# Kernel optimization log

Hardware: AMD Instinct MI355X
Metric: run time of the kernel (lower is better)

Reference implementation:

```python
import jax, jax.numpy as jnp
import numpy as np

KERNEL = 7  # neighborhood window (7x7)
NUM_HEADS = 4


def _window_idx(L, k):
    # NATTEN edge-clamped window start: each query attends to exactly k neighbors.
    starts = jnp.clip(jnp.arange(L) - k // 2, 0, L - k)  # [L]
    return starts[:, None] + jnp.arange(k)[None, :]       # [L, k]


def setup_inputs() -> dict:
    key = jax.random.key(0)
    k1, k2, k3, k4, k5 = jax.random.split(key, 5)
    B, H, W, D = 8, 64, 64, 128
    return {
        "x": jax.random.normal(k1, (B, H, W, D), dtype=jnp.float32),
        "w_qkv": jax.random.normal(k2, (3 * D, D), dtype=jnp.float32) * 0.02,
        "b_qkv": jax.random.normal(k3, (3 * D,), dtype=jnp.float32) * 0.02,
        "w_proj": jax.random.normal(k4, (D, D), dtype=jnp.float32) * 0.02,
        "b_proj": jax.random.normal(k5, (D,), dtype=jnp.float32) * 0.02,
    }


def reference(x, w_qkv, b_qkv, w_proj, b_proj):
    B, H, W, D = x.shape
    nh, k = NUM_HEADS, KERNEL
    hd = D // nh
    scale = hd ** -0.5

    # QKV projection -> [3, B, nh, H, W, hd]
    qkv = x @ w_qkv.T + b_qkv
    qkv = qkv.reshape(B, H, W, 3, nh, hd).transpose(3, 0, 4, 1, 2, 5)
    q, kk, v = qkv[0], qkv[1], qkv[2]

    idx_h = _window_idx(H, k)  # [H, k]
    idx_w = _window_idx(W, k)  # [W, k]
    IH = idx_h[:, None, :, None]  # [H,1,k,1]
    IW = idx_w[None, :, None, :]  # [1,W,1,k]

    # Gather local K/V neighborhoods: [B, nh, H, W, k, k, hd] -> [B, nh, H, W, k*k, hd]
    kn = kk[:, :, IH, IW, :].reshape(B, nh, H, W, k * k, hd)
    vn = v[:, :, IH, IW, :].reshape(B, nh, H, W, k * k, hd)

    attn = jnp.einsum('bhxyd,bhxynd->bhxyn', q * scale, kn)
    attn = jax.nn.softmax(attn, axis=-1)
    out = jnp.einsum('bhxyn,bhxynd->bhxyd', attn, vn)

    out = out.transpose(0, 2, 3, 1, 4).reshape(B, H, W, D)
    return out @ w_proj.T + b_proj
```

## Files before the change

kernel.cpp:

```cpp
#include <hip/hip_runtime.h>
#include <hip/hip_bf16.h>

#define BB 8
#define HH 64
#define WW 64
#define DD 128
#define NH 4
#define HD 32
#define KS 7
#define TS 8
#define HALO 14

typedef __attribute__((ext_vector_type(8))) short short8v;
typedef __attribute__((ext_vector_type(4))) short short4v;
typedef __attribute__((ext_vector_type(4))) float f32x4;
typedef unsigned short bf16_t;

__device__ inline bf16_t f2bf(float f) {
  __hip_bfloat16 h = __float2bfloat16(f);
  return *reinterpret_cast<bf16_t*>(&h);
}

__global__ __launch_bounds__(256) void qkv_mfma(
    const float* __restrict__ x, const float* __restrict__ w,
    const float* __restrict__ bqkv,
    bf16_t* __restrict__ q, bf16_t* __restrict__ k, bf16_t* __restrict__ v) {
  __shared__ __align__(16) short smA[64 * 128];
  __shared__ __align__(16) short smB[128 * 128];
  const int tid = threadIdx.x;
  const int m_tile = blockIdx.x;
  const int n_tile = blockIdx.y;

  const float* Ab = x + (size_t)m_tile * 64 * 128;
  const float* Bb = w + (size_t)n_tile * 128 * 128;
#pragma unroll
  for (int i = 0; i < 4; i++) {
    int idx = tid + i * 256;
    int r = idx >> 4, p = idx & 15;
    const float* ap = Ab + r * 128 + p * 8;
    float4 a0 = *(const float4*)ap;
    float4 a1 = *(const float4*)(ap + 4);
    short8v s;
    s[0] = f2bf(a0.x); s[1] = f2bf(a0.y); s[2] = f2bf(a0.z); s[3] = f2bf(a0.w);
    s[4] = f2bf(a1.x); s[5] = f2bf(a1.y); s[6] = f2bf(a1.z); s[7] = f2bf(a1.w);
    *(short8v*)((char*)smA + ((r * 256 + p * 16) ^ ((r & 7) << 4))) = s;
  }
#pragma unroll
  for (int i = 0; i < 8; i++) {
    int idx = tid + i * 256;
    int r = idx >> 4, p = idx & 15;
    const float* bp_ = Bb + r * 128 + p * 8;
    float4 b0 = *(const float4*)bp_;
    float4 b1 = *(const float4*)(bp_ + 4);
    short8v t;
    t[0] = f2bf(b0.x); t[1] = f2bf(b0.y); t[2] = f2bf(b0.z); t[3] = f2bf(b0.w);
    t[4] = f2bf(b1.x); t[5] = f2bf(b1.y); t[6] = f2bf(b1.z); t[7] = f2bf(b1.w);
    *(short8v*)((char*)smB + ((r * 256 + p * 16) ^ ((r & 7) << 4))) = t;
  }
  __syncthreads();

  const int lane = tid & 63, wid = tid >> 6;
  const int wm = wid >> 1, wn = wid & 1;
  const int l15 = lane & 15, l4 = lane >> 4;

  f32x4 acc[2][4] = {};
  const int rowA0 = wm * 32 + l15;
  const int rowB0 = wn * 64 + l15;
  const int swzA = (rowA0 & 7) << 4;
  const int swzB = (rowB0 & 7) << 4;

#pragma unroll
  for (int ks = 0; ks < 4; ks++) {
    const int cb = ks * 64 + l4 * 16;
    short8v a[2], b[4];
#pragma unroll
    for (int mi = 0; mi < 2; mi++)
      a[mi] = *(const short8v*)((const char*)smA +
                ((((rowA0 + mi * 16) * 256) + cb) ^ swzA));
#pragma unroll
    for (int nj = 0; nj < 4; nj++)
      b[nj] = *(const short8v*)((const char*)smB +
                ((((rowB0 + nj * 16) * 256) + cb) ^ swzB));
#pragma unroll
    for (int mi = 0; mi < 2; mi++)
#pragma unroll
      for (int nj = 0; nj < 4; nj++)
        acc[mi][nj] = __builtin_amdgcn_mfma_f32_16x16x32_bf16(a[mi], b[nj], acc[mi][nj], 0, 0, 0);
  }

  __syncthreads();
  short* smC = smA;
  const float qscale = 0.17677669529663687f;
  const float sc = (n_tile == 0) ? qscale : 1.f;
#pragma unroll
  for (int nj = 0; nj < 4; nj++) {
    const int n_local = wn * 64 + nj * 16 + l15;
    const float bias = bqkv[n_tile * 128 + n_local];
#pragma unroll
    for (int mi = 0; mi < 2; mi++) {
#pragma unroll
      for (int r = 0; r < 4; r++) {
        const int m = wm * 32 + mi * 16 + l4 * 4 + r;
        *(bf16_t*)((char*)smC + ((m * 256 + n_local * 2) ^ ((m & 7) << 4))) =
            f2bf((acc[mi][nj][r] + bias) * sc);
      }
    }
  }
  __syncthreads();

  const int bblk = m_tile >> 6;
  bf16_t* outp = (n_tile == 0) ? q : ((n_tile == 1) ? k : v);
#pragma unroll
  for (int i = 0; i < 4; i++) {
    const int idx = i * 256 + tid;
    const int h = idx >> 8;
    const int rem = idx & 255;
    const int m = rem >> 2, c = rem & 3;
    short8v t8 = *(const short8v*)((const char*)smC +
        ((m * 256 + h * 64 + c * 16) ^ ((m & 7) << 4)));
    const int pix = (m_tile * 64 + m) & 4095;
    *(short8v*)(outp + ((size_t)(bblk * 4 + h)) * 131072 + (size_t)pix * 32 + c * 8) = t8;
  }
}

__global__ __launch_bounds__(256) void attn_mfma(
    const bf16_t* __restrict__ q, const bf16_t* __restrict__ k,
    const bf16_t* __restrict__ v, bf16_t* __restrict__ ao) {
  __shared__ __align__(16) char vtb[16384];

  const int tile = blockIdx.x;
  const int tx = tile >> 3, ty = tile & 7;
  const int head = blockIdx.y, bb = blockIdx.z;
  const size_t bh = ((size_t)bb * NH + head) * 4096;
  const bf16_t* kb = k + bh * HD;
  const bf16_t* vb = v + bh * HD;
  const bf16_t* qb = q + bh * HD;
  const int rstart = min(max(tx * TS - 3, 0), HH - HALO);
  const int cstart = min(max(ty * TS - 3, 0), WW - HALO);
  const int tid = threadIdx.x;
  const int lane = tid & 63, wid = tid >> 6;
  const int l15 = lane & 15, h4 = lane >> 4;

  short8v qf;
  int qx, qy;
  {
    const int pit = wid * 16 + l15;
    qx = tx * TS + (pit >> 3);
    qy = ty * TS + (pit & 7);
    qf = *(const short8v*)(qb + ((size_t)(qx * WW + qy)) * HD + h4 * 8);
  }
  const int wx0 = min(max(qx - 3, 0), HH - KS) - rstart;
  const int wy0 = min(max(qy - 3, 0), WW - KS) - cstart;

  const int x0 = tx * TS + wid * 2;
  const int w0 = min(max(x0 - 3, 0), HH - KS) - rstart;
  const int base = min(w0 & ~1, 4);

  short4v vl[4][2];
#pragma unroll
  for (int t = 0; t < 4; t++) {
    const int idx = tid + t * 256;
    if (idx < 784) {
      const int pp = idx >> 3, c = idx & 7;
      const int pr = pp / 7, pc2 = (pp % 7) * 2;
      const size_t g = ((size_t)((rstart + pr) * WW + (cstart + pc2))) * HD + c * 4;
      vl[t][0] = *(const short4v*)(vb + g);
      vl[t][1] = *(const short4v*)(vb + g + HD);
    }
  }

  f32x4 acc[10];
  const f32x4 zf = {0.f, 0.f, 0.f, 0.f};
  const int kcol = cstart + min(l15, 13);
#pragma unroll
  for (int ch = 0; ch < 2; ch++) {
    short8v kf[5];
#pragma unroll
    for (int i = 0; i < 5; i++) {
      const int pr = rstart + base + ch * 5 + i;
      kf[i] = *(const short8v*)(kb + ((size_t)(pr * WW + kcol)) * HD + h4 * 8);
    }
    __builtin_amdgcn_s_setprio(1);
#pragma unroll
    for (int i = 0; i < 5; i++)
      acc[ch * 5 + i] = __builtin_amdgcn_mfma_f32_16x16x32_bf16(kf[i], qf, zf, 0, 0, 0);
    __builtin_amdgcn_s_setprio(0);
  }

#pragma unroll
  for (int t = 0; t < 4; t++) {
    const int idx = tid + t * 256;
    if (idx < 784) {
      const int pp = idx >> 3, c = idx & 7;
      const int pr = pp / 7, pc2 = (pp % 7) * 2;
      const int pos0 = ((pr >> 1) << 5) + ((pc2 >> 2) << 3) + ((pr & 1) << 2) + (pc2 & 3);
#pragma unroll
      for (int j = 0; j < 4; j++) {
        const int d = c * 4 + j;
        const unsigned pk2 = (unsigned)(unsigned short)vl[t][0][j] |
                             ((unsigned)(unsigned short)vl[t][1][j] << 16);
        *(unsigned*)(vtb + ((d * 512 + pos0 * 2) ^ ((d & 7) << 4))) = pk2;
      }
    }
  }
  for (int idx = tid; idx < 512; idx += 256) {
    const int d = idx >> 4, pr = idx & 15;
    if (pr < 14) {
      const int pos = ((pr >> 1) << 5) + 24 + ((pr & 1) << 2) + 2;
      *(unsigned*)(vtb + ((d * 512 + pos * 2) ^ ((d & 7) << 4))) = 0u;
    }
  }
  __syncthreads();

  bool cv[4];
#pragma unroll
  for (int r = 0; r < 4; r++) cv[r] = ((unsigned)(h4 * 4 + r - wy0) < 7u);
  float sum = 0.f;
#pragma unroll
  for (int nt = 0; nt < 10; nt++) {
    const bool rv = ((unsigned)(base + nt - wx0) < 7u);
#pragma unroll
    for (int r = 0; r < 4; r++) {
      const float p = (rv && cv[r]) ? __expf(acc[nt][r]) : 0.f;
      acc[nt][r] = p;
      sum += p;
    }
  }
  sum += __shfl_xor(sum, 16);
  sum += __shfl_xor(sum, 32);
  const float inv = 1.f / sum;

  f32x4 o0 = zf, o1 = zf;
  const int swzv = (l15 & 7) << 4;
  const int cbase = (base >> 1) * 64;
  __builtin_amdgcn_s_setprio(1);
#pragma unroll
  for (int kc = 0; kc < 5; kc++) {
    union { unsigned u[4]; short8v s; } pa;
    pa.u[0] = (unsigned)f2bf(acc[2 * kc][0] * inv) |
              ((unsigned)f2bf(acc[2 * kc][1] * inv) << 16);
    pa.u[1] = (unsigned)f2bf(acc[2 * kc][2] * inv) |
              ((unsigned)f2bf(acc[2 * kc][3] * inv) << 16);
    pa.u[2] = (unsigned)f2bf(acc[2 * kc + 1][0] * inv) |
              ((unsigned)f2bf(acc[2 * kc + 1][1] * inv) << 16);
    pa.u[3] = (unsigned)f2bf(acc[2 * kc + 1][2] * inv) |
              ((unsigned)f2bf(acc[2 * kc + 1][3] * inv) << 16);
    const int boff = cbase + kc * 64 + h4 * 16;
    short8v vb0 = *(const short8v*)(vtb + ((l15 * 512 + boff) ^ swzv));
    short8v vb1 = *(const short8v*)(vtb + (((l15 + 16) * 512 + boff) ^ swzv));
    o0 = __builtin_amdgcn_mfma_f32_16x16x32_bf16(pa.s, vb0, o0, 0, 0, 0);
    o1 = __builtin_amdgcn_mfma_f32_16x16x32_bf16(pa.s, vb1, o1, 0, 0, 0);
  }
  __builtin_amdgcn_s_setprio(0);

#pragma unroll
  for (int r = 0; r < 4; r++) {
    const int pit = wid * 16 + h4 * 4 + r;
    const int x = tx * TS + (pit >> 3), y = ty * TS + (pit & 7);
    bf16_t* op = ao + ((size_t)bb * 4096 + x * WW + y) * DD + head * HD;
    op[l15]      = (bf16_t)f2bf(o0[r]);
    op[l15 + 16] = (bf16_t)f2bf(o1[r]);
  }
}

__global__ __launch_bounds__(256) void proj_mfma(
    const bf16_t* __restrict__ aob, const float* __restrict__ wp,
    const float* __restrict__ bp, float* __restrict__ out) {
  __shared__ __align__(16) char plds[49152];
  short* smA = (short*)plds;
  short* smB = (short*)(plds + 16384);
  const int tid = threadIdx.x;
  const int m_tile = blockIdx.x;

  const bf16_t* Ab = aob + (size_t)m_tile * 64 * 128;
#pragma unroll
  for (int i = 0; i < 4; i++) {
    int idx = tid + i * 256;
    int r = idx >> 4, p = idx & 15;
    short8v s = *(const short8v*)(Ab + r * 128 + p * 8);
    *(short8v*)((char*)smA + ((r * 256 + p * 16) ^ ((r & 7) << 4))) = s;
  }
#pragma unroll
  for (int i = 0; i < 8; i++) {
    int idx = tid + i * 256;
    int r = idx >> 4, p = idx & 15;
    const float* bp_ = wp + r * 128 + p * 8;
    float4 b0 = *(const float4*)bp_;
    float4 b1 = *(const float4*)(bp_ + 4);
    short8v t;
    t[0] = f2bf(b0.x); t[1] = f2bf(b0.y); t[2] = f2bf(b0.z); t[3] = f2bf(b0.w);
    t[4] = f2bf(b1.x); t[5] = f2bf(b1.y); t[6] = f2bf(b1.z); t[7] = f2bf(b1.w);
    *(short8v*)((char*)smB + ((r * 256 + p * 16) ^ ((r & 7) << 4))) = t;
  }
  __syncthreads();

  const int lane = tid & 63, wid = tid >> 6;
  const int wm = wid >> 1, wn = wid & 1;
  const int l15 = lane & 15, l4 = lane >> 4;

  f32x4 acc[2][4] = {};
  const int rowA0 = wm * 32 + l15;
  const int rowB0 = wn * 64 + l15;
  const int swzA = (rowA0 & 7) << 4;
  const int swzB = (rowB0 & 7) << 4;

#pragma unroll
  for (int ks = 0; ks < 4; ks++) {
    const int cb = ks * 64 + l4 * 16;
    short8v a[2], b[4];
#pragma unroll
    for (int mi = 0; mi < 2; mi++)
      a[mi] = *(const short8v*)((const char*)smA +
                ((((rowA0 + mi * 16) * 256) + cb) ^ swzA));
#pragma unroll
    for (int nj = 0; nj < 4; nj++)
      b[nj] = *(const short8v*)((const char*)smB +
                ((((rowB0 + nj * 16) * 256) + cb) ^ swzB));
#pragma unroll
    for (int mi = 0; mi < 2; mi++)
#pragma unroll
      for (int nj = 0; nj < 4; nj++)
        acc[mi][nj] = __builtin_amdgcn_mfma_f32_16x16x32_bf16(a[mi], b[nj], acc[mi][nj], 0, 0, 0);
  }

  __syncthreads();
  char* smC = plds + 16384;
#pragma unroll
  for (int nj = 0; nj < 4; nj++) {
    const int n = wn * 64 + nj * 16 + l15;
    const float bias = bp[n];
#pragma unroll
    for (int mi = 0; mi < 2; mi++) {
#pragma unroll
      for (int r = 0; r < 4; r++) {
        const int m = wm * 32 + mi * 16 + l4 * 4 + r;
        *(float*)(smC + ((m * 512 + n * 4) ^ ((m & 7) << 5))) = acc[mi][nj][r] + bias;
      }
    }
  }
  __syncthreads();

#pragma unroll
  for (int i = 0; i < 8; i++) {
    const int idx = i * 256 + tid;
    const int m = idx >> 5, c = idx & 31;
    float4 t = *(const float4*)(smC + ((m * 512 + c * 16) ^ ((m & 7) << 5)));
    *(float4*)(out + (size_t)(m_tile * 64 + m) * DD + c * 4) = t;
  }
}

extern "C" void kernel_launch(void* const* d_in, const int* in_sizes, int n_in,
                              void* d_out, int out_size, void* d_ws, size_t ws_size,
                              hipStream_t stream) {
  const float* x      = (const float*)d_in[0];
  const float* w_qkv  = (const float*)d_in[1];
  const float* b_qkv  = (const float*)d_in[2];
  const float* w_proj = (const float*)d_in[3];
  const float* b_proj = (const float*)d_in[4];
  float* out = (float*)d_out;

  const size_t per = (size_t)BB * NH * HH * WW * HD;
  bf16_t* q  = (bf16_t*)d_ws;
  bf16_t* k  = q + per;
  bf16_t* v  = k + per;
  bf16_t* ao = v + per;

  qkv_mfma<<<dim3(512, 3), dim3(256), 0, stream>>>(x, w_qkv, b_qkv, q, k, v);
  attn_mfma<<<dim3(64, NH, BB), dim3(256), 0, stream>>>(q, k, v, ao);
  proj_mfma<<<dim3(512), dim3(256), 0, stream>>>(ao, w_proj, b_proj, out);
}
```

Measured before the change: 41.08 us.

## Fuse neighborhood attention with output projection, looping heads per block

Merges the attention and projection kernels into one. Each block now handles an 8x8 spatial tile across all four heads in sequence, keeps the per-head outputs in registers, stages them into LDS as a 64x128 bf16 tile, and runs the projection GEMM directly. This drops the intermediate attention-output round trip through global memory and one kernel launch. The cost is a 4x smaller grid (512 blocks), serial head processing with extra barriers inside each block, higher register pressure, and 48KB of LDS per block, which may lower occupancy.

```diff
diff --git a/kernel.cpp b/kernel.cpp
--- a/kernel.cpp
+++ b/kernel.cpp
@@ -123,163 +123,24 @@
   }
 }
 
-__global__ __launch_bounds__(256) void attn_mfma(
+__global__ __launch_bounds__(256) void attn_proj_fused(
     const bf16_t* __restrict__ q, const bf16_t* __restrict__ k,
-    const bf16_t* __restrict__ v, bf16_t* __restrict__ ao) {
-  __shared__ __align__(16) char vtb[16384];
+    const bf16_t* __restrict__ v, const float* __restrict__ wp,
+    const float* __restrict__ bpj, float* __restrict__ out) {
+  __shared__ __align__(16) char lds[49152];
+  char* vtb = lds;
+  short* wpb = (short*)(lds + 16384);
 
   const int tile = blockIdx.x;
   const int tx = tile >> 3, ty = tile & 7;
-  const int head = blockIdx.y, bb = blockIdx.z;
-  const size_t bh = ((size_t)bb * NH + head) * 4096;
-  const bf16_t* kb = k + bh * HD;
-  const bf16_t* vb = v + bh * HD;
-  const bf16_t* qb = q + bh * HD;
+  const int bb = blockIdx.y;
   const int rstart = min(max(tx * TS - 3, 0), HH - HALO);
   const int cstart = min(max(ty * TS - 3, 0), WW - HALO);
   const int tid = threadIdx.x;
   const int lane = tid & 63, wid = tid >> 6;
   const int l15 = lane & 15, h4 = lane >> 4;
-
-  short8v qf;
-  int qx, qy;
-  {
-    const int pit = wid * 16 + l15;
-    qx = tx * TS + (pit >> 3);
-    qy = ty * TS + (pit & 7);
-    qf = *(const short8v*)(qb + ((size_t)(qx * WW + qy)) * HD + h4 * 8);
-  }
-  const int wx0 = min(max(qx - 3, 0), HH - KS) - rstart;
-  const int wy0 = min(max(qy - 3, 0), WW - KS) - cstart;
-
-  const int x0 = tx * TS + wid * 2;
-  const int w0 = min(max(x0 - 3, 0), HH - KS) - rstart;
-  const int base = min(w0 & ~1, 4);
-
-  short4v vl[4][2];
-#pragma unroll
-  for (int t = 0; t < 4; t++) {
-    const int idx = tid + t * 256;
-    if (idx < 784) {
-      const int pp = idx >> 3, c = idx & 7;
-      const int pr = pp / 7, pc2 = (pp % 7) * 2;
-      const size_t g = ((size_t)((rstart + pr) * WW + (cstart + pc2))) * HD + c * 4;
-      vl[t][0] = *(const short4v*)(vb + g);
-      vl[t][1] = *(const short4v*)(vb + g + HD);
-    }
-  }
-
-  f32x4 acc[10];
-  const f32x4 zf = {0.f, 0.f, 0.f, 0.f};
-  const int kcol = cstart + min(l15, 13);
-#pragma unroll
-  for (int ch = 0; ch < 2; ch++) {
-    short8v kf[5];
-#pragma unroll
-    for (int i = 0; i < 5; i++) {
-      const int pr = rstart + base + ch * 5 + i;
-      kf[i] = *(const short8v*)(kb + ((size_t)(pr * WW + kcol)) * HD + h4 * 8);
-    }
-    __builtin_amdgcn_s_setprio(1);
-#pragma unroll
-    for (int i = 0; i < 5; i++)
-      acc[ch * 5 + i] = __builtin_amdgcn_mfma_f32_16x16x32_bf16(kf[i], qf, zf, 0, 0, 0);
-    __builtin_amdgcn_s_setprio(0);
-  }
-
-#pragma unroll
-  for (int t = 0; t < 4; t++) {
-    const int idx = tid + t * 256;
-    if (idx < 784) {
-      const int pp = idx >> 3, c = idx & 7;
-      const int pr = pp / 7, pc2 = (pp % 7) * 2;
-      const int pos0 = ((pr >> 1) << 5) + ((pc2 >> 2) << 3) + ((pr & 1) << 2) + (pc2 & 3);
-#pragma unroll
-      for (int j = 0; j < 4; j++) {
-        const int d = c * 4 + j;
-        const unsigned pk2 = (unsigned)(unsigned short)vl[t][0][j] |
-                             ((unsigned)(unsigned short)vl[t][1][j] << 16);
-        *(unsigned*)(vtb + ((d * 512 + pos0 * 2) ^ ((d & 7) << 4))) = pk2;
-      }
-    }
-  }
-  for (int idx = tid; idx < 512; idx += 256) {
-    const int d = idx >> 4, pr = idx & 15;
-    if (pr < 14) {
-      const int pos = ((pr >> 1) << 5) + 24 + ((pr & 1) << 2) + 2;
-      *(unsigned*)(vtb + ((d * 512 + pos * 2) ^ ((d & 7) << 4))) = 0u;
-    }
-  }
-  __syncthreads();
-
-  bool cv[4];
-#pragma unroll
-  for (int r = 0; r < 4; r++) cv[r] = ((unsigned)(h4 * 4 + r - wy0) < 7u);
-  float sum = 0.f;
-#pragma unroll
-  for (int nt = 0; nt < 10; nt++) {
-    const bool rv = ((unsigned)(base + nt - wx0) < 7u);
-#pragma unroll
-    for (int r = 0; r < 4; r++) {
-      const float p = (rv && cv[r]) ? __expf(acc[nt][r]) : 0.f;
-      acc[nt][r] = p;
-      sum += p;
-    }
-  }
-  sum += __shfl_xor(sum, 16);
-  sum += __shfl_xor(sum, 32);
-  const float inv = 1.f / sum;
-
-  f32x4 o0 = zf, o1 = zf;
-  const int swzv = (l15 & 7) << 4;
-  const int cbase = (base >> 1) * 64;
-  __builtin_amdgcn_s_setprio(1);
-#pragma unroll
-  for (int kc = 0; kc < 5; kc++) {
-    union { unsigned u[4]; short8v s; } pa;
-    pa.u[0] = (unsigned)f2bf(acc[2 * kc][0] * inv) |
-              ((unsigned)f2bf(acc[2 * kc][1] * inv) << 16);
-    pa.u[1] = (unsigned)f2bf(acc[2 * kc][2] * inv) |
-              ((unsigned)f2bf(acc[2 * kc][3] * inv) << 16);
-    pa.u[2] = (unsigned)f2bf(acc[2 * kc + 1][0] * inv) |
-              ((unsigned)f2bf(acc[2 * kc + 1][1] * inv) << 16);
-    pa.u[3] = (unsigned)f2bf(acc[2 * kc + 1][2] * inv) |
-              ((unsigned)f2bf(acc[2 * kc + 1][3] * inv) << 16);
-    const int boff = cbase + kc * 64 + h4 * 16;
-    short8v vb0 = *(const short8v*)(vtb + ((l15 * 512 + boff) ^ swzv));
-    short8v vb1 = *(const short8v*)(vtb + (((l15 + 16) * 512 + boff) ^ swzv));
-    o0 = __builtin_amdgcn_mfma_f32_16x16x32_bf16(pa.s, vb0, o0, 0, 0, 0);
-    o1 = __builtin_amdgcn_mfma_f32_16x16x32_bf16(pa.s, vb1, o1, 0, 0, 0);
-  }
-  __builtin_amdgcn_s_setprio(0);
-
-#pragma unroll
-  for (int r = 0; r < 4; r++) {
-    const int pit = wid * 16 + h4 * 4 + r;
-    const int x = tx * TS + (pit >> 3), y = ty * TS + (pit & 7);
-    bf16_t* op = ao + ((size_t)bb * 4096 + x * WW + y) * DD + head * HD;
-    op[l15]      = (bf16_t)f2bf(o0[r]);
-    op[l15 + 16] = (bf16_t)f2bf(o1[r]);
-  }
-}
-
-__global__ __launch_bounds__(256) void proj_mfma(
-    const bf16_t* __restrict__ aob, const float* __restrict__ wp,
-    const float* __restrict__ bp, float* __restrict__ out) {
-  __shared__ __align__(16) char plds[49152];
-  short* smA = (short*)plds;
-  short* smB = (short*)(plds + 16384);
-  const int tid = threadIdx.x;
-  const int m_tile = blockIdx.x;
-
-  const bf16_t* Ab = aob + (size_t)m_tile * 64 * 128;
-#pragma unroll
-  for (int i = 0; i < 4; i++) {
-    int idx = tid + i * 256;
-    int r = idx >> 4, p = idx & 15;
-    short8v s = *(const short8v*)(Ab + r * 128 + p * 8);
-    *(short8v*)((char*)smA + ((r * 256 + p * 16) ^ ((r & 7) << 4))) = s;
-  }
+  const size_t bb4 = (size_t)bb * 4;
+
 #pragma unroll
   for (int i = 0; i < 8; i++) {
     int idx = tid + i * 256;
@@ -290,15 +151,159 @@
     short8v t;
     t[0] = f2bf(b0.x); t[1] = f2bf(b0.y); t[2] = f2bf(b0.z); t[3] = f2bf(b0.w);
     t[4] = f2bf(b1.x); t[5] = f2bf(b1.y); t[6] = f2bf(b1.z); t[7] = f2bf(b1.w);
-    *(short8v*)((char*)smB + ((r * 256 + p * 16) ^ ((r & 7) << 4))) = t;
-  }
-  __syncthreads();
-
-  const int lane = tid & 63, wid = tid >> 6;
+    *(short8v*)((char*)wpb + ((r * 256 + p * 16) ^ ((r & 7) << 4))) = t;
+  }
+
+  int qx, qy;
+  {
+    const int pit = wid * 16 + l15;
+    qx = tx * TS + (pit >> 3);
+    qy = ty * TS + (pit & 7);
+  }
+  const size_t qoff = (size_t)(qx * WW + qy) * HD + h4 * 8;
+  const int wx0 = min(max(qx - 3, 0), HH - KS) - rstart;
+  const int wy0 = min(max(qy - 3, 0), WW - KS) - cstart;
+  const int x0 = tx * TS + wid * 2;
+  const int w0 = min(max(x0 - 3, 0), HH - KS) - rstart;
+  const int base = min(w0 & ~1, 4);
+  bool cv[4];
+#pragma unroll
+  for (int r = 0; r < 4; r++) cv[r] = ((unsigned)(h4 * 4 + r - wy0) < 7u);
+  const int kcol = cstart + min(l15, 13);
+  const f32x4 zf = {0.f, 0.f, 0.f, 0.f};
+
+  short8v qf[4];
+#pragma unroll
+  for (int h = 0; h < 4; h++)
+    qf[h] = *(const short8v*)(q + (bb4 + h) * 131072 + qoff);
+
+  unsigned oph[4][4];
+
+#pragma unroll
+  for (int h = 0; h < 4; h++) {
+    const bf16_t* kb = k + (bb4 + h) * 131072;
+    const bf16_t* vb = v + (bb4 + h) * 131072;
+
+    short4v vl[4][2];
+#pragma unroll
+    for (int t = 0; t < 4; t++) {
+      const int idx = tid + t * 256;
+      if (idx < 784) {
+        const int pp = idx >> 3, c = idx & 7;
+        const int pr = pp / 7, pc2 = (pp % 7) * 2;
+        const size_t g = ((size_t)((rstart + pr) * WW + (cstart + pc2))) * HD + c * 4;
+        vl[t][0] = *(const short4v*)(vb + g);
+        vl[t][1] = *(const short4v*)(vb + g + HD);
+      }
+    }
+
+    f32x4 acc[10];
+#pragma unroll
+    for (int ch = 0; ch < 2; ch++) {
+      short8v kf[5];
+#pragma unroll
+      for (int i = 0; i < 5; i++) {
+        const int pr = rstart + base + ch * 5 + i;
+        kf[i] = *(const short8v*)(kb + ((size_t)(pr * WW + kcol)) * HD + h4 * 8);
+      }
+      __builtin_amdgcn_s_setprio(1);
+#pragma unroll
+      for (int i = 0; i < 5; i++)
+        acc[ch * 5 + i] = __builtin_amdgcn_mfma_f32_16x16x32_bf16(kf[i], qf[h], zf, 0, 0, 0);
+      __builtin_amdgcn_s_setprio(0);
+    }
+
+    if (h > 0) __syncthreads();
+
+#pragma unroll
+    for (int t = 0; t < 4; t++) {
+      const int idx = tid + t * 256;
+      if (idx < 784) {
+        const int pp = idx >> 3, c = idx & 7;
+        const int pr = pp / 7, pc2 = (pp % 7) * 2;
+        const int pos0 = ((pr >> 1) << 5) + ((pc2 >> 2) << 3) + ((pr & 1) << 2) + (pc2 & 3);
+#pragma unroll
+        for (int j = 0; j < 4; j++) {
+          const int d = c * 4 + j;
+          const unsigned pk2 = (unsigned)(unsigned short)vl[t][0][j] |
+                               ((unsigned)(unsigned short)vl[t][1][j] << 16);
+          *(unsigned*)(vtb + ((d * 512 + pos0 * 2) ^ ((d & 7) << 4))) = pk2;
+        }
+      }
+    }
+    if (h == 0) {
+      for (int idx = tid; idx < 512; idx += 256) {
+        const int d = idx >> 4, pr = idx & 15;
+        if (pr < 14) {
+          const int pos = ((pr >> 1) << 5) + 24 + ((pr & 1) << 2) + 2;
+          *(unsigned*)(vtb + ((d * 512 + pos * 2) ^ ((d & 7) << 4))) = 0u;
+        }
+      }
+    }
+    __syncthreads();
+
+    float sum = 0.f;
+#pragma unroll
+    for (int nt = 0; nt < 10; nt++) {
+      const bool rv = ((unsigned)(base + nt - wx0) < 7u);
+#pragma unroll
+      for (int r = 0; r < 4; r++) {
+        const float p = (rv && cv[r]) ? __expf(acc[nt][r]) : 0.f;
+        acc[nt][r] = p;
+        sum += p;
+      }
+    }
+    sum += __shfl_xor(sum, 16);
+    sum += __shfl_xor(sum, 32);
+    const float inv = 1.f / sum;
+
+    f32x4 o0 = zf, o1 = zf;
+    const int swzv = (l15 & 7) << 4;
+    const int cbase = (base >> 1) * 64;
+    __builtin_amdgcn_s_setprio(1);
+#pragma unroll
+    for (int kc = 0; kc < 5; kc++) {
+      union { unsigned u[4]; short8v s; } pa;
+      pa.u[0] = (unsigned)f2bf(acc[2 * kc][0] * inv) |
+                ((unsigned)f2bf(acc[2 * kc][1] * inv) << 16);
+      pa.u[1] = (unsigned)f2bf(acc[2 * kc][2] * inv) |
+                ((unsigned)f2bf(acc[2 * kc][3] * inv) << 16);
+      pa.u[2] = (unsigned)f2bf(acc[2 * kc + 1][0] * inv) |
+                ((unsigned)f2bf(acc[2 * kc + 1][1] * inv) << 16);
+      pa.u[3] = (unsigned)f2bf(acc[2 * kc + 1][2] * inv) |
+                ((unsigned)f2bf(acc[2 * kc + 1][3] * inv) << 16);
+      const int boff = cbase + kc * 64 + h4 * 16;
+      short8v vb0 = *(const short8v*)(vtb + ((l15 * 512 + boff) ^ swzv));
+      short8v vb1 = *(const short8v*)(vtb + (((l15 + 16) * 512 + boff) ^ swzv));
+      o0 = __builtin_amdgcn_mfma_f32_16x16x32_bf16(pa.s, vb0, o0, 0, 0, 0);
+      o1 = __builtin_amdgcn_mfma_f32_16x16x32_bf16(pa.s, vb1, o1, 0, 0, 0);
+    }
+    __builtin_amdgcn_s_setprio(0);
+
+    oph[h][0] = (unsigned)f2bf(o0[0]) | ((unsigned)f2bf(o0[1]) << 16);
+    oph[h][1] = (unsigned)f2bf(o0[2]) | ((unsigned)f2bf(o0[3]) << 16);
+    oph[h][2] = (unsigned)f2bf(o1[0]) | ((unsigned)f2bf(o1[1]) << 16);
+    oph[h][3] = (unsigned)f2bf(o1[2]) | ((unsigned)f2bf(o1[3]) << 16);
+  }
+  __syncthreads();
+
+#pragma unroll
+  for (int h = 0; h < 4; h++) {
+#pragma unroll
+    for (int j = 0; j < 4; j++) {
+      const unsigned u = oph[h][j];
+      const int row0 = wid * 16 + h4 * 4 + (j & 1) * 2;
+      const int d = h * 32 + (j >> 1) * 16 + l15;
+      *(bf16_t*)(vtb + ((row0 * 256 + d * 2) ^ ((row0 & 7) << 4))) = (bf16_t)(u & 0xFFFFu);
+      const int row1 = row0 + 1;
+      *(bf16_t*)(vtb + ((row1 * 256 + d * 2) ^ ((row1 & 7) << 4))) = (bf16_t)(u >> 16);
+    }
+  }
+  __syncthreads();
+
   const int wm = wid >> 1, wn = wid & 1;
-  const int l15 = lane & 15, l4 = lane >> 4;
-
-  f32x4 acc[2][4] = {};
+  const int l4 = lane >> 4;
+  f32x4 pacc[2][4] = {};
   const int rowA0 = wm * 32 + l15;
   const int rowB0 = wn * 64 + l15;
   const int swzA = (rowA0 & 7) << 4;
@@ -310,42 +315,45 @@
     short8v a[2], b[4];
 #pragma unroll
     for (int mi = 0; mi < 2; mi++)
-      a[mi] = *(const short8v*)((const char*)smA +
-                ((((rowA0 + mi * 16) * 256) + cb) ^ swzA));
+      a[mi] = *(const short8v*)(vtb + ((((rowA0 + mi * 16) * 256) + cb) ^ swzA));
 #pragma unroll
     for (int nj = 0; nj < 4; nj++)
-      b[nj] = *(const short8v*)((const char*)smB +
+      b[nj] = *(const short8v*)((const char*)wpb +
                 ((((rowB0 + nj * 16) * 256) + cb) ^ swzB));
+    __builtin_amdgcn_s_setprio(1);
 #pragma unroll
     for (int mi = 0; mi < 2; mi++)
 #pragma unroll
       for (int nj = 0; nj < 4; nj++)
-        acc[mi][nj] = __builtin_amdgcn_mfma_f32_16x16x32_bf16(a[mi], b[nj], acc[mi][nj], 0, 0, 0);
-  }
-
-  __syncthreads();
-  char* smC = plds + 16384;
+        pacc[mi][nj] = __builtin_amdgcn_mfma_f32_16x16x32_bf16(a[mi], b[nj], pacc[mi][nj], 0, 0, 0);
+    __builtin_amdgcn_s_setprio(0);
+  }
+
+  __syncthreads();
+  char* smC = lds + 16384;
 #pragma unroll
   for (int nj = 0; nj < 4; nj++) {
     const int n = wn * 64 + nj * 16 + l15;
-    const float bias = bp[n];
+    const float bias = bpj[n];
 #pragma unroll
     for (int mi = 0; mi < 2; mi++) {
 #pragma unroll
       for (int r = 0; r < 4; r++) {
         const int m = wm * 32 + mi * 16 + l4 * 4 + r;
-        *(float*)(smC + ((m * 512 + n * 4) ^ ((m & 7) << 5))) = acc[mi][nj][r] + bias;
-      }
-    }
-  }
-  __syncthreads();
-
+        *(float*)(smC + ((m * 512 + n * 4) ^ ((m & 7) << 5))) = pacc[mi][nj][r] + bias;
+      }
+    }
+  }
+  __syncthreads();
+
+  float* obase = out + ((size_t)bb * 4096 + (size_t)(tx * TS) * WW + ty * TS) * DD;
 #pragma unroll
   for (int i = 0; i < 8; i++) {
     const int idx = i * 256 + tid;
     const int m = idx >> 5, c = idx & 31;
     float4 t = *(const float4*)(smC + ((m * 512 + c * 16) ^ ((m & 7) << 5)));
-    *(float4*)(out + (size_t)(m_tile * 64 + m) * DD + c * 4) = t;
+    const size_t grow = (size_t)(m >> 3) * WW + (m & 7);
+    *(float4*)(obase + grow * DD + c * 4) = t;
   }
 }
 
@@ -360,12 +368,10 @@
   float* out = (float*)d_out;
 
   const size_t per = (size_t)BB * NH * HH * WW * HD;
-  bf16_t* q  = (bf16_t*)d_ws;
-  bf16_t* k  = q + per;
-  bf16_t* v  = k + per;
-  bf16_t* ao = v + per;
+  bf16_t* q = (bf16_t*)d_ws;
+  bf16_t* k = q + per;
+  bf16_t* v = k + per;
 
   qkv_mfma<<<dim3(512, 3), dim3(256), 0, stream>>>(x, w_qkv, b_qkv, q, k, v);
-  attn_mfma<<<dim3(64, NH, BB), dim3(256), 0, stream>>>(q, k, v, ao);
-  proj_mfma<<<dim3(512), dim3(256), 0, stream>>>(ao, w_proj, b_proj, out);
+  attn_proj_fused<<<dim3(64, BB), dim3(256), 0, stream>>>(q, k, v, w_proj, b_proj, out);
 }
```

Result: no change. 40.83 us (-0.6%).
